# Kernel optimization log

Hardware: AMD Instinct MI355X
Metric: run time of the kernel (lower is better)

The kernel has to match this reference:

```python
import jax, jax.numpy as jnp
import numpy as np

B, S, D, H, L = 8, 1024, 512, 8, 6
DK = D // H
DFF = 4 * D
EPS = 1e-5
SCALE = float(np.sqrt(DK))  # torch: sqrt(d_k)


def setup_inputs() -> dict:
    key = jax.random.key(0)
    ks = jax.random.split(key, 10)
    init = lambda k, shape: jax.random.normal(k, shape, jnp.float32) * 0.02
    return {
        "x": jax.random.normal(ks[0], (B, S, D), jnp.float32),
        "qkv_w": init(ks[1], (L, D, 3 * D)),
        "qkv_b": init(ks[2], (L, 3 * D)),
        "out_w": init(ks[3], (L, D, D)),
        "out_b": init(ks[4], (L, D)),
        "ln1_g": jnp.ones((L, D), jnp.float32),
        "ln1_b": jnp.zeros((L, D), jnp.float32),
        "mlp_w1": init(ks[5], (L, D, DFF)),
        "mlp_b1": init(ks[6], (L, DFF)),
        "mlp_w2": init(ks[7], (L, DFF, D)),
        "mlp_b2": init(ks[8], (L, D)),
        "ln2_g": jnp.ones((L, D), jnp.float32),
        "ln2_b": jnp.zeros((L, D), jnp.float32),
    }


def _layer_norm(x, g, b):
    m = jnp.mean(x, axis=-1, keepdims=True)
    v = jnp.var(x, axis=-1, keepdims=True)  # biased var, matches torch LayerNorm
    return (x - m) * jax.lax.rsqrt(v + EPS) * g + b


def reference(x, qkv_w, qkv_b, out_w, out_b, ln1_g, ln1_b,
              mlp_w1, mlp_b1, mlp_w2, mlp_b2, ln2_g, ln2_b):
    b, s, d = x.shape
    causal = jnp.tril(jnp.ones((s, s), dtype=bool))  # [S,S]
    for i in range(L):
        # --- causal self-attention, post-LN residual (dropout = eval identity) ---
        qkv = x @ qkv_w[i] + qkv_b[i]                      # [B,S,3D]
        q, k, v = jnp.split(qkv, 3, axis=-1)
        q = q.reshape(b, s, H, DK)
        k = k.reshape(b, s, H, DK)
        v = v.reshape(b, s, H, DK)
        att = jnp.einsum('bqhd,bkhd->bhqk', q, k) / SCALE  # [B,H,S,S]
        att = jnp.where(causal, att, -jnp.inf)
        att = jax.nn.softmax(att, axis=-1)
        o = jnp.einsum('bhqk,bkhd->bqhd', att, v).reshape(b, s, d)
        x = _layer_norm(o @ out_w[i] + out_b[i] + x, ln1_g[i], ln1_b[i])
        # --- MLP, post-LN residual ---
        h = jax.nn.relu(x @ mlp_w1[i] + mlp_b1[i]) @ mlp_w2[i] + mlp_b2[i]
        x = _layer_norm(x + h, ln2_g[i], ln2_b[i])
    return x
```

## Files before the change

### kernel.cpp

```cpp
#include <hip/hip_runtime.h>
#include <math.h>

#define Bn   8
#define Sn   1024
#define Dn   512
#define Hn   8
#define DKn  64
#define Ln   6
#define DFFn 2048
#define Mn   (Bn * Sn)

typedef __bf16 bf16x8 __attribute__((ext_vector_type(8)));
typedef __bf16 bf16x4 __attribute__((ext_vector_type(4)));
typedef __bf16 bf16x2 __attribute__((ext_vector_type(2)));
typedef float  f32x4  __attribute__((ext_vector_type(4)));

__device__ __forceinline__ void gl_lds16(const void* g, void* l) {
    __builtin_amdgcn_global_load_lds(
        (const __attribute__((address_space(1))) void*)g,
        (__attribute__((address_space(3))) void*)l, 16, 0, 0);
}

__global__ __launch_bounds__(256) void k_cast_bf16(const float* __restrict__ in,
                                                   __bf16* __restrict__ out, int n) {
    int i = blockIdx.x * 256 + threadIdx.x;
    if (i < n) out[i] = (__bf16)in[i];
}

__global__ __launch_bounds__(256) void k_trans_all(
    const float* __restrict__ qkv_w, const float* __restrict__ out_w,
    const float* __restrict__ w1, const float* __restrict__ w2,
    __bf16* __restrict__ Wq, __bf16* __restrict__ Wo,
    __bf16* __restrict__ W1o, __bf16* __restrict__ W2o)
{
    const int lay = blockIdx.x / 3072;
    const int t   = blockIdx.x % 3072;
    const float* src; __bf16* dst; int K, N, n0, k0;
    if (t < 768)       { src = qkv_w + (size_t)lay * Dn * 3 * Dn; dst = Wq  + (size_t)lay * 3 * Dn * Dn;
                         K = 512;  N = 1536; int u = t;        n0 = (u % 48) * 32; k0 = (u / 48) * 32; }
    else if (t < 1024) { src = out_w + (size_t)lay * Dn * Dn;     dst = Wo  + (size_t)lay * Dn * Dn;
                         K = 512;  N = 512;  int u = t - 768;  n0 = (u % 16) * 32; k0 = (u / 16) * 32; }
    else if (t < 2048) { src = w1 + (size_t)lay * Dn * DFFn;      dst = W1o + (size_t)lay * DFFn * Dn;
                         K = 512;  N = 2048; int u = t - 1024; n0 = (u % 64) * 32; k0 = (u / 64) * 32; }
    else               { src = w2 + (size_t)lay * DFFn * Dn;      dst = W2o + (size_t)lay * Dn * DFFn;
                         K = 2048; N = 512;  int u = t - 2048; n0 = (u % 16) * 32; k0 = (u / 16) * 32; }

    __shared__ float tt[32][33];
    const int tx = threadIdx.x, ty = threadIdx.y;
    #pragma unroll
    for (int r = 0; r < 4; r++)
        tt[ty + 8 * r][tx] = src[(size_t)(k0 + ty + 8 * r) * N + n0 + tx];
    __syncthreads();
    #pragma unroll
    for (int r = 0; r < 4; r++)
        dst[(size_t)(n0 + ty + 8 * r) * K + k0 + tx] = (__bf16)tt[tx][ty + 8 * r];
}

template <int RELU, int OUTBF, int JT, int VW, int BK>
__global__ __launch_bounds__(256) void k_gemm_mfma(
    const __bf16* __restrict__ A, const __bf16* __restrict__ Bt,
    const float* __restrict__ bias, void* __restrict__ Cout,
    __bf16* __restrict__ Vt, int M, int N, int K, int NBX)
{
    constexpr int BN = JT * 32;
    constexpr int UR = BK / 8;
    constexpr int HC = BK / 32;
    __shared__ __bf16 As[128][BK];
    __shared__ __bf16 Bs[BN][BK];
    const int tid  = threadIdx.x;
    const int lane = tid & 63;
    const int wave = tid >> 6;
    const int wy   = wave >> 1, wx = wave & 1;
    const int m16  = lane & 15, quad = lane >> 4;

    const int cpx = gridDim.x >> 3;
    const int id  = (blockIdx.x & 7) * cpx + (blockIdx.x >> 3);
    const int bm  = (id / NBX) * 128;
    const int bn  = (id % NBX) * BN;

    f32x4 acc[4][JT];
    #pragma unroll
    for (int i = 0; i < 4; i++)
        #pragma unroll
        for (int j = 0; j < JT; j++)
            acc[i][j] = (f32x4){0.f, 0.f, 0.f, 0.f};

    const __bf16* Ap = A  + (size_t)bm * K;
    const __bf16* Bp = Bt + (size_t)bn * K;

    int sw[HC];
    #pragma unroll
    for (int hc = 0; hc < HC; hc++)
        sw[hc] = ((quad + 4 * hc) ^ (m16 & (UR - 1))) * 8;

    for (int k0 = 0; k0 < K; k0 += BK) {
        __syncthreads();
        #pragma unroll
        for (int c = 0; c < UR / 2; c++) {
            int lin = tid + c * 256;
            int row = lin / UR, uu = lin % UR;
            int su  = (uu ^ (row & (UR - 1))) << 3;
            gl_lds16(Ap + (size_t)row * K + k0 + su, (void*)(&As[0][0] + lin * 8));
        }
        #pragma unroll
        for (int c = 0; c < (JT * UR) / 8; c++) {
            int lin = tid + c * 256;
            int row = lin / UR, uu = lin % UR;
            int su  = (uu ^ (row & (UR - 1))) << 3;
            gl_lds16(Bp + (size_t)row * K + k0 + su, (void*)(&Bs[0][0] + lin * 8));
        }
        __syncthreads();

        bf16x8 af[4][HC], bfr[JT][HC];
        #pragma unroll
        for (int i = 0; i < 4; i++)
            #pragma unroll
            for (int hc = 0; hc < HC; hc++)
                af[i][hc] = *(const bf16x8*)&As[wy * 64 + i * 16 + m16][sw[hc]];
        #pragma unroll
        for (int j = 0; j < JT; j++)
            #pragma unroll
            for (int hc = 0; hc < HC; hc++)
                bfr[j][hc] = *(const bf16x8*)&Bs[wx * JT * 16 + j * 16 + m16][sw[hc]];
        #pragma unroll
        for (int hc = 0; hc < HC; hc++)
            #pragma unroll
            for (int i = 0; i < 4; i++)
                #pragma unroll
                for (int j = 0; j < JT; j++)
                    acc[i][j] = __builtin_amdgcn_mfma_f32_16x16x32_bf16(
                        af[i][hc], bfr[j][hc], acc[i][j], 0, 0, 0);
    }

    float*  Cf = (float*)Cout;
    __bf16* Cb = (__bf16*)Cout;
    #pragma unroll
    for (int i = 0; i < 4; i++) {
        const int row0 = bm + wy * 64 + i * 16 + quad * 4;
        #pragma unroll
        for (int j = 0; j < JT; j++) {
            const int col = bn + wx * JT * 16 + j * 16 + m16;
            const float bv = bias[col];
            float vv[4];
            #pragma unroll
            for (int r = 0; r < 4; r++) {
                float v = acc[i][j][r] + bv;
                if (RELU) v = fmaxf(v, 0.f);
                vv[r] = v;
                if (OUTBF) Cb[(size_t)(row0 + r) * N + col] = (__bf16)v;
                else       Cf[(size_t)(row0 + r) * N + col] = v;
            }
            if (VW && col >= 1024) {
                const int cc = col - 1024;
                const int bb = row0 >> 10, ss = row0 & 1023;
                bf16x4 pv;
                #pragma unroll
                for (int r = 0; r < 4; r++) pv[r] = (__bf16)vv[r];
                *(bf16x4*)&Vt[((size_t)(bb * Hn + (cc >> 6)) * DKn + (cc & 63)) * Sn + ss] = pv;
            }
        }
    }
}

__device__ __forceinline__ void softmax_update_sw(
    f32x4 sv[4], float& m, float& l, f32x4 acc[4],
    bool diag, int wave16, int quad, int m16,
    __bf16 (*Pw)[72], bf16x8& pf0, bf16x8& pf1)
{
    const float SC = 0.125f * 1.44269504089f;
    float pmax = -1e30f;
    #pragma unroll
    for (int j = 0; j < 4; j++)
        #pragma unroll
        for (int r = 0; r < 4; r++) {
            float v = sv[j][r] * SC;
            if (diag && (j * 16 + quad * 4 + r) > (wave16 + m16)) v = -1e30f;
            sv[j][r] = v;
            pmax = fmaxf(pmax, v);
        }
    pmax = fmaxf(pmax, __shfl_xor(pmax, 16));
    pmax = fmaxf(pmax, __shfl_xor(pmax, 32));

    if (__any((int)(pmax > m + 11.54f))) {
        float mn = fmaxf(m, pmax);
        float al = __builtin_amdgcn_exp2f(m - mn);
        m = mn;
        l *= al;
        float alr[4];
        #pragma unroll
        for (int r = 0; r < 4; r++) alr[r] = __shfl(al, quad * 4 + r, 16);
        #pragma unroll
        for (int j = 0; j < 4; j++)
            #pragma unroll
            for (int r = 0; r < 4; r++) acc[j][r] *= alr[r];
    }

    float rs = 0.f;
    #pragma unroll
    for (int j = 0; j < 4; j++) {
        bf16x4 pw;
        #pragma unroll
        for (int r = 0; r < 4; r++) {
            float p = __builtin_amdgcn_exp2f(sv[j][r] - m);
            rs += p;
            pw[r] = (__bf16)p;
        }
        *(bf16x4*)&Pw[m16][j * 16 + quad * 4] = pw;
    }
    rs += __shfl_xor(rs, 16);
    rs += __shfl_xor(rs, 32);
    l += rs;

    pf0 = *(const bf16x8*)&Pw[m16][quad * 8];
    pf1 = *(const bf16x8*)&Pw[m16][32 + quad * 8];
}

__global__ __launch_bounds__(512, 4) void k_attn_mfma(
    const __bf16* __restrict__ qkv, const __bf16* __restrict__ Vt,
    __bf16* __restrict__ o)
{
    const int id = blockIdx.x;
    const int u  = id >> 6;
    const int pr = (u < 4) ? u : 11 - u;
    const int b  = (id >> 3) & 7;
    const int h  = id & 7;
    const int tid  = threadIdx.x;
    const int lane = tid & 63, wave = tid >> 6;
    const int m16  = lane & 15, quad = lane >> 4;
    const int isB  = wave >> 2;
    const int wave16 = (wave & 3) * 16;
    const int qtA  = pr, qtB = 15 - pr;
    const int qt   = isB ? qtB : qtA;

    __shared__ __bf16 Kb[2][64][64];
    __shared__ __bf16 Vb[2][64][64];
    __shared__ __bf16 Ps[8][16][72];

    const __bf16* base = qkv + (size_t)b * Sn * 1536 + h * DKn;
    const __bf16* vtb  = Vt + (size_t)(b * Hn + h) * DKn * Sn;
    __bf16 (*Pw)[72] = Ps[wave];

    const int sw0 = ((quad    ) ^ (m16 & 7)) * 8;
    const int sw1 = ((quad + 4) ^ (m16 & 7)) * 8;

    const int srow = tid >> 3;
    const int ssu  = ((tid & 7) ^ (srow & 7)) * 8;

    #define STAGE(KT, BB)                                                       \
        {                                                                       \
            gl_lds16(base + (size_t)((KT) * 64 + srow) * 1536 + 512 + ssu,      \
                     (void*)(&Kb[BB][0][0] + tid * 8));                         \
            gl_lds16(vtb + (size_t)srow * Sn + (KT) * 64 + ssu,                 \
                     (void*)(&Vb[BB][0][0] + tid * 8));                         \
        }

    STAGE(0, 0);

    bf16x8 q0, q1;
    {
        const __bf16* qa = base + (size_t)(qt * 64 + wave16 + m16) * 1536 + quad * 8;
        q0 = *(const bf16x8*)qa; q1 = *(const bf16x8*)(qa + 32);
    }

    float m = -1e30f, l = 0.f;
    f32x4 acc[4];
    #pragma unroll
    for (int r = 0; r < 4; r++) acc[r] = (f32x4){0.f, 0.f, 0.f, 0.f};

    for (int kt = 0; kt <= qtB; kt++) {
        const int buf = kt & 1;
        if (kt < qtB) {
            STAGE(kt + 1, buf ^ 1);
            asm volatile("s_waitcnt vmcnt(2)" ::: "memory");
        } else {
            asm volatile("s_waitcnt vmcnt(0)" ::: "memory");
        }
        __builtin_amdgcn_s_barrier();

        if (isB || kt <= qtA) {
            f32x4 sv[4];
            __builtin_amdgcn_s_setprio(1);
            #pragma unroll
            for (int j = 0; j < 4; j++) {
                const int rk = j * 16 + m16;
                bf16x8 kf0 = *(const bf16x8*)&Kb[buf][rk][sw0];
                bf16x8 kf1 = *(const bf16x8*)&Kb[buf][rk][sw1];
                f32x4 s = (f32x4){0.f, 0.f, 0.f, 0.f};
                s = __builtin_amdgcn_mfma_f32_16x16x32_bf16(kf0, q0, s, 0, 0, 0);
                s = __builtin_amdgcn_mfma_f32_16x16x32_bf16(kf1, q1, s, 0, 0, 0);
                sv[j] = s;
            }
            __builtin_amdgcn_s_setprio(0);

            bf16x8 vf[4][2];
            #pragma unroll
            for (int jd = 0; jd < 4; jd++) {
                const int rv = jd * 16 + m16;
                vf[jd][0] = *(const bf16x8*)&Vb[buf][rv][sw0];
                vf[jd][1] = *(const bf16x8*)&Vb[buf][rv][sw1];
            }

            bf16x8 p0, p1;
            softmax_update_sw(sv, m, l, acc, kt == qt, wave16, quad, m16, Pw, p0, p1);

            __builtin_amdgcn_s_setprio(1);
            #pragma unroll
            for (int jd = 0; jd < 4; jd++) {
                acc[jd] = __builtin_amdgcn_mfma_f32_16x16x32_bf16(p0, vf[jd][0], acc[jd], 0, 0, 0);
                acc[jd] = __builtin_amdgcn_mfma_f32_16x16x32_bf16(p1, vf[jd][1], acc[jd], 0, 0, 0);
            }
            __builtin_amdgcn_s_setprio(0);
        }

        asm volatile("s_waitcnt lgkmcnt(0)" ::: "memory");
        __builtin_amdgcn_s_barrier();
    }
    #undef STAGE

    float linv[4];
    #pragma unroll
    for (int r = 0; r < 4; r++) linv[r] = 1.0f / __shfl(l, quad * 4 + r, 16);
    #pragma unroll
    for (int jd = 0; jd < 4; jd++)
        #pragma unroll
        for (int r = 0; r < 4; r++) {
            const int row = b * Sn + qt * 64 + wave16 + quad * 4 + r;
            o[(size_t)row * Dn + h * DKn + jd * 16 + m16] = (__bf16)(acc[jd][r] * linv[r]);
        }
}

template <int FINAL>
__global__ __launch_bounds__(256) void k_residual_ln(
    const __bf16* __restrict__ t, __bf16* __restrict__ xb,
    const float* __restrict__ g, const float* __restrict__ be,
    float* __restrict__ outf)
{
    const int row  = (blockIdx.x << 2) | (threadIdx.x >> 6);
    const int lane = threadIdx.x & 63;
    const size_t base = (size_t)row * Dn + lane * 8;

    bf16x8 tv = *(const bf16x8*)&t[base];
    bf16x8 xv = *(const bf16x8*)&xb[base];
    float v[8];
    float s = 0.f;
    #pragma unroll
    for (int i = 0; i < 8; i++) {
        v[i] = (float)tv[i] + (float)xv[i];
        s += v[i];
    }
    #pragma unroll
    for (int off = 1; off < 64; off <<= 1) s += __shfl_xor(s, off);
    const float mean = s * (1.0f / Dn);

    float vs = 0.f;
    #pragma unroll
    for (int i = 0; i < 8; i++) {
        v[i] -= mean;
        vs += v[i] * v[i];
    }
    #pragma unroll
    for (int off = 1; off < 64; off <<= 1) vs += __shfl_xor(vs, off);
    const float inv = rsqrtf(vs * (1.0f / Dn) + 1e-5f);

    const f32x4 g0 = *(const f32x4*)&g[lane * 8];
    const f32x4 g1 = *(const f32x4*)&g[lane * 8 + 4];
    const f32x4 b0 = *(const f32x4*)&be[lane * 8];
    const f32x4 b1 = *(const f32x4*)&be[lane * 8 + 4];

    if (FINAL) {
        f32x4 o0, o1;
        #pragma unroll
        for (int i = 0; i < 4; i++) {
            o0[i] = v[i] * inv * g0[i] + b0[i];
            o1[i] = v[i + 4] * inv * g1[i] + b1[i];
        }
        *(f32x4*)&outf[base]     = o0;
        *(f32x4*)&outf[base + 4] = o1;
    } else {
        bf16x8 ov;
        #pragma unroll
        for (int i = 0; i < 4; i++) {
            ov[i]     = (__bf16)(v[i] * inv * g0[i] + b0[i]);
            ov[i + 4] = (__bf16)(v[i + 4] * inv * g1[i] + b1[i]);
        }
        *(bf16x8*)&xb[base] = ov;
    }
}

extern "C" void kernel_launch(void* const* d_in, const int* in_sizes, int n_in,
                              void* d_out, int out_size, void* d_ws, size_t ws_size,
                              hipStream_t stream)
{
    const float* x_in   = (const float*)d_in[0];
    const float* qkv_w  = (const float*)d_in[1];
    const float* qkv_b  = (const float*)d_in[2];
    const float* out_w  = (const float*)d_in[3];
    const float* out_b  = (const float*)d_in[4];
    const float* ln1_g  = (const float*)d_in[5];
    const float* ln1_b  = (const float*)d_in[6];
    const float* mlp_w1 = (const float*)d_in[7];
    const float* mlp_b1 = (const float*)d_in[8];
    const float* mlp_w2 = (const float*)d_in[9];
    const float* mlp_b2 = (const float*)d_in[10];
    const float* ln2_g  = (const float*)d_in[11];
    const float* ln2_b  = (const float*)d_in[12];

    char* p = (char*)d_ws;
    __bf16* Xb    = (__bf16*)p; p += (size_t)Mn * Dn * 2;
    __bf16* QKVb  = (__bf16*)p; p += (size_t)Mn * 3 * Dn * 2;
    __bf16* AOb   = (__bf16*)p; p += (size_t)Mn * Dn * 2;
    __bf16* Hb    = (__bf16*)p; p += (size_t)Mn * DFFn * 2;
    __bf16* BUF3b = (__bf16*)p; p += (size_t)Mn * Dn * 2;
    __bf16* Wq    = (__bf16*)p; p += (size_t)Ln * 3 * Dn * Dn * 2;
    __bf16* Wo    = (__bf16*)p; p += (size_t)Ln * Dn * Dn * 2;
    __bf16* W1    = (__bf16*)p; p += (size_t)Ln * DFFn * Dn * 2;
    __bf16* W2    = (__bf16*)p; p += (size_t)Ln * Dn * DFFn * 2;
    __bf16* Vt    = Hb;

    k_cast_bf16<<<(Mn * Dn) / 256, 256, 0, stream>>>(x_in, Xb, Mn * Dn);

    k_trans_all<<<Ln * 3072, dim3(32, 8), 0, stream>>>(
        qkv_w, out_w, mlp_w1, mlp_w2, Wq, Wo, W1, W2);

    for (int l = 0; l < Ln; l++) {
        const __bf16* Wql = Wq + (size_t)l * 3 * Dn * Dn;
        const __bf16* Wol = Wo + (size_t)l * Dn * Dn;
        const __bf16* W1l = W1 + (size_t)l * DFFn * Dn;
        const __bf16* W2l = W2 + (size_t)l * Dn * DFFn;

        k_gemm_mfma<0, 1, 4, 1, 64><<<768, 256, 0, stream>>>(
            Xb, Wql, qkv_b + (size_t)l * 3 * Dn, QKVb, Vt, Mn, 3 * Dn, Dn, 12);
        k_attn_mfma<<<512, 512, 0, stream>>>(QKVb, Vt, AOb);
        k_gemm_mfma<0, 1, 2, 0, 128><<<512, 256, 0, stream>>>(
            AOb, Wol, out_b + (size_t)l * Dn, BUF3b, nullptr, Mn, Dn, Dn, 8);
        k_residual_ln<0><<<Mn / 4, 256, 0, stream>>>(BUF3b, Xb,
            ln1_g + (size_t)l * Dn, ln1_b + (size_t)l * Dn, nullptr);
        k_gemm_mfma<1, 1, 4, 0, 64><<<1024, 256, 0, stream>>>(
            Xb, W1l, mlp_b1 + (size_t)l * DFFn, Hb, nullptr, Mn, DFFn, Dn, 16);
        k_gemm_mfma<0, 1, 2, 0, 128><<<512, 256, 0, stream>>>(
            Hb, W2l, mlp_b2 + (size_t)l * Dn, BUF3b, nullptr, Mn, Dn, DFFn, 8);
        if (l == Ln - 1)
            k_residual_ln<1><<<Mn / 4, 256, 0, stream>>>(BUF3b, Xb,
                ln2_g + (size_t)l * Dn, ln2_b + (size_t)l * Dn, (float*)d_out);
        else
            k_residual_ln<0><<<Mn / 4, 256, 0, stream>>>(BUF3b, Xb,
                ln2_g + (size_t)l * Dn, ln2_b + (size_t)l * Dn, nullptr);
    }
}
```

Before: 847.6 us.

## Double-buffer LDS staging with counted vmcnt in narrow GEMMs, skip redundant V stores

Replaces the BK template parameter with a DBUF flag. For the out-proj and MLP-down GEMMs (JT=2), the K-tile is reduced from 128 to 64 and two LDS buffers are used. The next tile's global-to-LDS loads are issued before computing the current one, and a counted s_waitcnt vmcnt(6) plus raw barriers overlap memory with MFMA work. Separately, the QKV GEMM no longer writes the V columns to the row-major QKV buffer, since they already go to the transposed Vt buffer. The risks are the hardcoded vmcnt count and halving the per-iteration K depth.

```diff
diff --git a/kernel.cpp b/kernel.cpp
--- a/kernel.cpp
+++ b/kernel.cpp
@@ -12,7 +12,6 @@
 
 typedef __bf16 bf16x8 __attribute__((ext_vector_type(8)));
 typedef __bf16 bf16x4 __attribute__((ext_vector_type(4)));
-typedef __bf16 bf16x2 __attribute__((ext_vector_type(2)));
 typedef float  f32x4  __attribute__((ext_vector_type(4)));
 
 __device__ __forceinline__ void gl_lds16(const void* g, void* l) {
@@ -56,17 +55,18 @@
         dst[(size_t)(n0 + ty + 8 * r) * K + k0 + tx] = (__bf16)tt[tx][ty + 8 * r];
 }
 
-template <int RELU, int OUTBF, int JT, int VW, int BK>
+template <int RELU, int OUTBF, int JT, int VW, int DBUF>
 __global__ __launch_bounds__(256) void k_gemm_mfma(
     const __bf16* __restrict__ A, const __bf16* __restrict__ Bt,
     const float* __restrict__ bias, void* __restrict__ Cout,
     __bf16* __restrict__ Vt, int M, int N, int K, int NBX)
 {
     constexpr int BN = JT * 32;
-    constexpr int UR = BK / 8;
-    constexpr int HC = BK / 32;
-    __shared__ __bf16 As[128][BK];
-    __shared__ __bf16 Bs[BN][BK];
+    constexpr int NBUF = DBUF ? 2 : 1;
+    constexpr int AC = 4;
+    constexpr int BC = JT;
+    __shared__ __bf16 As[NBUF][128][64];
+    __shared__ __bf16 Bs[NBUF][BN][64];
     const int tid  = threadIdx.x;
     const int lane = tid & 63;
     const int wave = tid >> 6;
@@ -88,48 +88,72 @@
     const __bf16* Ap = A  + (size_t)bm * K;
     const __bf16* Bp = Bt + (size_t)bn * K;
 
-    int sw[HC];
-    #pragma unroll
-    for (int hc = 0; hc < HC; hc++)
-        sw[hc] = ((quad + 4 * hc) ^ (m16 & (UR - 1))) * 8;
-
-    for (int k0 = 0; k0 < K; k0 += BK) {
-        __syncthreads();
-        #pragma unroll
-        for (int c = 0; c < UR / 2; c++) {
+    const int sw0 = ((quad    ) ^ (m16 & 7)) * 8;
+    const int sw1 = ((quad + 4) ^ (m16 & 7)) * 8;
+
+    auto stage = [&](int k0, int bb) {
+        #pragma unroll
+        for (int c = 0; c < AC; c++) {
             int lin = tid + c * 256;
-            int row = lin / UR, uu = lin % UR;
-            int su  = (uu ^ (row & (UR - 1))) << 3;
-            gl_lds16(Ap + (size_t)row * K + k0 + su, (void*)(&As[0][0] + lin * 8));
-        }
-        #pragma unroll
-        for (int c = 0; c < (JT * UR) / 8; c++) {
+            int row = lin >> 3, uu = lin & 7;
+            int su  = (uu ^ (row & 7)) << 3;
+            gl_lds16(Ap + (size_t)row * K + k0 + su, (void*)(&As[bb][0][0] + lin * 8));
+        }
+        #pragma unroll
+        for (int c = 0; c < BC; c++) {
             int lin = tid + c * 256;
-            int row = lin / UR, uu = lin % UR;
-            int su  = (uu ^ (row & (UR - 1))) << 3;
-            gl_lds16(Bp + (size_t)row * K + k0 + su, (void*)(&Bs[0][0] + lin * 8));
-        }
-        __syncthreads();
-
-        bf16x8 af[4][HC], bfr[JT][HC];
-        #pragma unroll
-        for (int i = 0; i < 4; i++)
-            #pragma unroll
-            for (int hc = 0; hc < HC; hc++)
-                af[i][hc] = *(const bf16x8*)&As[wy * 64 + i * 16 + m16][sw[hc]];
-        #pragma unroll
-        for (int j = 0; j < JT; j++)
-            #pragma unroll
-            for (int hc = 0; hc < HC; hc++)
-                bfr[j][hc] = *(const bf16x8*)&Bs[wx * JT * 16 + j * 16 + m16][sw[hc]];
-        #pragma unroll
-        for (int hc = 0; hc < HC; hc++)
+            int row = lin >> 3, uu = lin & 7;
+            int su  = (uu ^ (row & 7)) << 3;
+            gl_lds16(Bp + (size_t)row * K + k0 + su, (void*)(&Bs[bb][0][0] + lin * 8));
+        }
+    };
+
+    auto compute = [&](int bb) {
+        bf16x8 af[4][2], bfr[JT][2];
+        #pragma unroll
+        for (int i = 0; i < 4; i++) {
+            af[i][0] = *(const bf16x8*)&As[bb][wy * 64 + i * 16 + m16][sw0];
+            af[i][1] = *(const bf16x8*)&As[bb][wy * 64 + i * 16 + m16][sw1];
+        }
+        #pragma unroll
+        for (int j = 0; j < JT; j++) {
+            bfr[j][0] = *(const bf16x8*)&Bs[bb][wx * JT * 16 + j * 16 + m16][sw0];
+            bfr[j][1] = *(const bf16x8*)&Bs[bb][wx * JT * 16 + j * 16 + m16][sw1];
+        }
+        #pragma unroll
+        for (int hc = 0; hc < 2; hc++)
             #pragma unroll
             for (int i = 0; i < 4; i++)
                 #pragma unroll
                 for (int j = 0; j < JT; j++)
                     acc[i][j] = __builtin_amdgcn_mfma_f32_16x16x32_bf16(
                         af[i][hc], bfr[j][hc], acc[i][j], 0, 0, 0);
+    };
+
+    if constexpr (DBUF) {
+        static_assert(JT == 2, "counted vmcnt hardcodes 6 = 4A+2B chunks");
+        const int NS = K >> 6;
+        stage(0, 0);
+        for (int s = 0; s < NS; s++) {
+            const int buf = s & 1;
+            if (s + 1 < NS) {
+                stage((s + 1) << 6, buf ^ 1);
+                asm volatile("s_waitcnt vmcnt(6)" ::: "memory");
+            } else {
+                asm volatile("s_waitcnt vmcnt(0)" ::: "memory");
+            }
+            __builtin_amdgcn_s_barrier();
+            compute(buf);
+            asm volatile("s_waitcnt lgkmcnt(0)" ::: "memory");
+            __builtin_amdgcn_s_barrier();
+        }
+    } else {
+        for (int k0 = 0; k0 < K; k0 += 64) {
+            __syncthreads();
+            stage(k0, 0);
+            __syncthreads();
+            compute(0);
+        }
     }
 
     float*  Cf = (float*)Cout;
@@ -147,8 +171,10 @@
                 float v = acc[i][j][r] + bv;
                 if (RELU) v = fmaxf(v, 0.f);
                 vv[r] = v;
-                if (OUTBF) Cb[(size_t)(row0 + r) * N + col] = (__bf16)v;
-                else       Cf[(size_t)(row0 + r) * N + col] = v;
+                if (!VW || col < 1024) {
+                    if (OUTBF) Cb[(size_t)(row0 + r) * N + col] = (__bf16)v;
+                    else       Cf[(size_t)(row0 + r) * N + col] = v;
+                }
             }
             if (VW && col >= 1024) {
                 const int cc = col - 1024;
@@ -428,16 +454,16 @@
         const __bf16* W1l = W1 + (size_t)l * DFFn * Dn;
         const __bf16* W2l = W2 + (size_t)l * Dn * DFFn;
 
-        k_gemm_mfma<0, 1, 4, 1, 64><<<768, 256, 0, stream>>>(
+        k_gemm_mfma<0, 1, 4, 1, 0><<<768, 256, 0, stream>>>(
             Xb, Wql, qkv_b + (size_t)l * 3 * Dn, QKVb, Vt, Mn, 3 * Dn, Dn, 12);
         k_attn_mfma<<<512, 512, 0, stream>>>(QKVb, Vt, AOb);
-        k_gemm_mfma<0, 1, 2, 0, 128><<<512, 256, 0, stream>>>(
+        k_gemm_mfma<0, 1, 2, 0, 1><<<512, 256, 0, stream>>>(
             AOb, Wol, out_b + (size_t)l * Dn, BUF3b, nullptr, Mn, Dn, Dn, 8);
         k_residual_ln<0><<<Mn / 4, 256, 0, stream>>>(BUF3b, Xb,
             ln1_g + (size_t)l * Dn, ln1_b + (size_t)l * Dn, nullptr);
-        k_gemm_mfma<1, 1, 4, 0, 64><<<1024, 256, 0, stream>>>(
+        k_gemm_mfma<1, 1, 4, 0, 0><<<1024, 256, 0, stream>>>(
             Xb, W1l, mlp_b1 + (size_t)l * DFFn, Hb, nullptr, Mn, DFFn, Dn, 16);
-        k_gemm_mfma<0, 1, 2, 0, 128><<<512, 256, 0, stream>>>(
+        k_gemm_mfma<0, 1, 2, 0, 1><<<512, 256, 0, stream>>>(
             Hb, W2l, mlp_b2 + (size_t)l * Dn, BUF3b, nullptr, Mn, Dn, DFFn, 8);
         if (l == Ln - 1)
             k_residual_ln<1><<<Mn / 4, 256, 0, stream>>>(BUF3b, Xb,
```

Result: slower. 907.2 us (+7.0%).

## Split-K the MLP down-projection GEMM and fuse partial summation into LayerNorm

Applied to the files above, without the earlier changes.

The second MLP GEMM (K=2048, N=512) is split into two K halves across twice as many blocks. Each half writes an fp32 partial into scratch space reused from the QKV and attention-output buffers, and the residual LayerNorm kernel adds both partials. The aim is to raise block count and parallelism for a GEMM whose output tile grid is small. The cost is extra fp32 write and read traffic for the two partial buffers in place of a single bf16 output. The QKV GEMM also stops writing V columns to the row-major QKV buffer, since V is already stored transposed.

```diff
diff --git a/kernel.cpp b/kernel.cpp
--- a/kernel.cpp
+++ b/kernel.cpp
@@ -12,7 +12,6 @@
 
 typedef __bf16 bf16x8 __attribute__((ext_vector_type(8)));
 typedef __bf16 bf16x4 __attribute__((ext_vector_type(4)));
-typedef __bf16 bf16x2 __attribute__((ext_vector_type(2)));
 typedef float  f32x4  __attribute__((ext_vector_type(4)));
 
 __device__ __forceinline__ void gl_lds16(const void* g, void* l) {
@@ -56,7 +55,7 @@
         dst[(size_t)(n0 + ty + 8 * r) * K + k0 + tx] = (__bf16)tt[tx][ty + 8 * r];
 }
 
-template <int RELU, int OUTBF, int JT, int VW, int BK>
+template <int RELU, int OUTBF, int JT, int VW, int BK, int SPLITK>
 __global__ __launch_bounds__(256) void k_gemm_mfma(
     const __bf16* __restrict__ A, const __bf16* __restrict__ Bt,
     const float* __restrict__ bias, void* __restrict__ Cout,
@@ -74,9 +73,16 @@
     const int m16  = lane & 15, quad = lane >> 4;
 
     const int cpx = gridDim.x >> 3;
-    const int id  = (blockIdx.x & 7) * cpx + (blockIdx.x >> 3);
+    int id = (blockIdx.x & 7) * cpx + (blockIdx.x >> 3);
+    int sk = 0;
+    if constexpr (SPLITK) {
+        const int half = gridDim.x >> 1;
+        if (id >= half) { sk = 1; id -= half; }
+    }
     const int bm  = (id / NBX) * 128;
     const int bn  = (id % NBX) * BN;
+    const int KL   = SPLITK ? (K >> 1) : K;
+    const int koff = SPLITK ? sk * KL : 0;
 
     f32x4 acc[4][JT];
     #pragma unroll
@@ -85,15 +91,15 @@
         for (int j = 0; j < JT; j++)
             acc[i][j] = (f32x4){0.f, 0.f, 0.f, 0.f};
 
-    const __bf16* Ap = A  + (size_t)bm * K;
-    const __bf16* Bp = Bt + (size_t)bn * K;
+    const __bf16* Ap = A  + (size_t)bm * K + koff;
+    const __bf16* Bp = Bt + (size_t)bn * K + koff;
 
     int sw[HC];
     #pragma unroll
     for (int hc = 0; hc < HC; hc++)
         sw[hc] = ((quad + 4 * hc) ^ (m16 & (UR - 1))) * 8;
 
-    for (int k0 = 0; k0 < K; k0 += BK) {
+    for (int k0 = 0; k0 < KL; k0 += BK) {
         __syncthreads();
         #pragma unroll
         for (int c = 0; c < UR / 2; c++) {
@@ -132,7 +138,7 @@
                         af[i][hc], bfr[j][hc], acc[i][j], 0, 0, 0);
     }
 
-    float*  Cf = (float*)Cout;
+    float*  Cf = (float*)Cout + (SPLITK ? (size_t)sk * Mn * Dn : 0);
     __bf16* Cb = (__bf16*)Cout;
     #pragma unroll
     for (int i = 0; i < 4; i++) {
@@ -140,15 +146,17 @@
         #pragma unroll
         for (int j = 0; j < JT; j++) {
             const int col = bn + wx * JT * 16 + j * 16 + m16;
-            const float bv = bias[col];
+            const float bv = (SPLITK && sk) ? 0.f : bias[col];
             float vv[4];
             #pragma unroll
             for (int r = 0; r < 4; r++) {
                 float v = acc[i][j][r] + bv;
                 if (RELU) v = fmaxf(v, 0.f);
                 vv[r] = v;
-                if (OUTBF) Cb[(size_t)(row0 + r) * N + col] = (__bf16)v;
-                else       Cf[(size_t)(row0 + r) * N + col] = v;
+                if (!VW || col < 1024) {
+                    if (OUTBF) Cb[(size_t)(row0 + r) * N + col] = (__bf16)v;
+                    else       Cf[(size_t)(row0 + r) * N + col] = v;
+                }
             }
             if (VW && col >= 1024) {
                 const int cc = col - 1024;
@@ -329,9 +337,9 @@
         }
 }
 
-template <int FINAL>
+template <int FINAL, int SPLIT>
 __global__ __launch_bounds__(256) void k_residual_ln(
-    const __bf16* __restrict__ t, __bf16* __restrict__ xb,
+    const void* __restrict__ t_, __bf16* __restrict__ xb,
     const float* __restrict__ g, const float* __restrict__ be,
     float* __restrict__ outf)
 {
@@ -339,15 +347,27 @@
     const int lane = threadIdx.x & 63;
     const size_t base = (size_t)row * Dn + lane * 8;
 
-    bf16x8 tv = *(const bf16x8*)&t[base];
     bf16x8 xv = *(const bf16x8*)&xb[base];
     float v[8];
     float s = 0.f;
-    #pragma unroll
-    for (int i = 0; i < 8; i++) {
-        v[i] = (float)tv[i] + (float)xv[i];
-        s += v[i];
-    }
+    if constexpr (SPLIT) {
+        const float* t0 = (const float*)t_;
+        const float* t1 = t0 + (size_t)Mn * Dn;
+        f32x4 a0 = *(const f32x4*)&t0[base], a1 = *(const f32x4*)&t0[base + 4];
+        f32x4 c0 = *(const f32x4*)&t1[base], c1 = *(const f32x4*)&t1[base + 4];
+        #pragma unroll
+        for (int i = 0; i < 4; i++) {
+            v[i]     = a0[i] + c0[i] + (float)xv[i];
+            v[i + 4] = a1[i] + c1[i] + (float)xv[i + 4];
+        }
+    } else {
+        const __bf16* tb = (const __bf16*)t_;
+        bf16x8 tv = *(const bf16x8*)&tb[base];
+        #pragma unroll
+        for (int i = 0; i < 8; i++) v[i] = (float)tv[i] + (float)xv[i];
+    }
+    #pragma unroll
+    for (int i = 0; i < 8; i++) s += v[i];
     #pragma unroll
     for (int off = 1; off < 64; off <<= 1) s += __shfl_xor(s, off);
     const float mean = s * (1.0f / Dn);
@@ -416,6 +436,7 @@
     __bf16* W1    = (__bf16*)p; p += (size_t)Ln * DFFn * Dn * 2;
     __bf16* W2    = (__bf16*)p; p += (size_t)Ln * Dn * DFFn * 2;
     __bf16* Vt    = Hb;
+    float*  T01   = (float*)QKVb;
 
     k_cast_bf16<<<(Mn * Dn) / 256, 256, 0, stream>>>(x_in, Xb, Mn * Dn);
 
@@ -428,22 +449,22 @@
         const __bf16* W1l = W1 + (size_t)l * DFFn * Dn;
         const __bf16* W2l = W2 + (size_t)l * Dn * DFFn;
 
-        k_gemm_mfma<0, 1, 4, 1, 64><<<768, 256, 0, stream>>>(
+        k_gemm_mfma<0, 1, 4, 1, 64, 0><<<768, 256, 0, stream>>>(
             Xb, Wql, qkv_b + (size_t)l * 3 * Dn, QKVb, Vt, Mn, 3 * Dn, Dn, 12);
         k_attn_mfma<<<512, 512, 0, stream>>>(QKVb, Vt, AOb);
-        k_gemm_mfma<0, 1, 2, 0, 128><<<512, 256, 0, stream>>>(
+        k_gemm_mfma<0, 1, 2, 0, 128, 0><<<512, 256, 0, stream>>>(
             AOb, Wol, out_b + (size_t)l * Dn, BUF3b, nullptr, Mn, Dn, Dn, 8);
-        k_residual_ln<0><<<Mn / 4, 256, 0, stream>>>(BUF3b, Xb,
+        k_residual_ln<0, 0><<<Mn / 4, 256, 0, stream>>>(BUF3b, Xb,
             ln1_g + (size_t)l * Dn, ln1_b + (size_t)l * Dn, nullptr);
-        k_gemm_mfma<1, 1, 4, 0, 64><<<1024, 256, 0, stream>>>(
+        k_gemm_mfma<1, 1, 4, 0, 64, 0><<<1024, 256, 0, stream>>>(
             Xb, W1l, mlp_b1 + (size_t)l * DFFn, Hb, nullptr, Mn, DFFn, Dn, 16);
-        k_gemm_mfma<0, 1, 2, 0, 128><<<512, 256, 0, stream>>>(
-            Hb, W2l, mlp_b2 + (size_t)l * Dn, BUF3b, nullptr, Mn, Dn, DFFn, 8);
+        k_gemm_mfma<0, 0, 2, 0, 128, 1><<<1024, 256, 0, stream>>>(
+            Hb, W2l, mlp_b2 + (size_t)l * Dn, T01, nullptr, Mn, Dn, DFFn, 8);
         if (l == Ln - 1)
-            k_residual_ln<1><<<Mn / 4, 256, 0, stream>>>(BUF3b, Xb,
+            k_residual_ln<1, 1><<<Mn / 4, 256, 0, stream>>>(T01, Xb,
                 ln2_g + (size_t)l * Dn, ln2_b + (size_t)l * Dn, (float*)d_out);
         else
-            k_residual_ln<0><<<Mn / 4, 256, 0, stream>>>(BUF3b, Xb,
+            k_residual_ln<0, 1><<<Mn / 4, 256, 0, stream>>>(T01, Xb,
                 ln2_g + (size_t)l * Dn, ln2_b + (size_t)l * Dn, nullptr);
     }
 }
```

Result: slower. 932.4 us (+10.0%).
